# Optimization experiments

Hardware: AMD Instinct MI355X
Metric: run time of the kernel (lower is better)

Reference implementation:

```python
import jax, jax.numpy as jnp
import numpy as np

N = 8192
DIMS = 128
HID = 64
NEG = -9e15


def setup_inputs() -> dict:
    key = jax.random.key(0)
    k_adj, k_h, k_w1, k_w2 = jax.random.split(key, 4)
    graph_info = (jax.random.uniform(k_adj, (N, N)) < 0.01).astype(jnp.float32)
    h = jax.random.normal(k_h, (N, DIMS), dtype=jnp.float32)
    # xavier-normal-ish init for the 2-layer scoring MLP (dims -> 64 -> 1)
    W1 = jax.random.normal(k_w1, (DIMS, HID), dtype=jnp.float32) * np.sqrt(2.0 / (DIMS + HID))
    b1 = jnp.zeros((HID,), dtype=jnp.float32)
    W2 = jax.random.normal(k_w2, (HID, 1), dtype=jnp.float32) * np.sqrt(2.0 / (HID + 1))
    b2 = jnp.zeros((1,), dtype=jnp.float32)
    return {"graph_info": graph_info, "h": h, "W1": W1, "b1": b1, "W2": W2, "b2": b2}


def reference(graph_info, h, W1, b1, W2, b2):
    # per-node MLP score: e_j for every node j  -> [N, 1]
    e = jnp.dot(jnp.maximum(jnp.dot(h, W1) + b1, 0.0), W2) + b2
    # e.transpose().repeat(N,1): row i sees scores of all columns j -> broadcast [1, N]
    scores = e[:, 0][None, :]
    # mask non-edges with large negative, softmax over neighbors (dim=-1)
    att = jnp.where(graph_info > 0, scores, jnp.float32(NEG))
    att = jax.nn.softmax(att, axis=-1)
    out = jnp.dot(att, h)  # [N, dims] aggregation
    # sum_flag == 1: rescale each row by its degree (diagflat(num) @ h)
    num = jnp.sum(graph_info, axis=-1)  # [N]
    out = num[:, None] * out
    return out
```

## Files before the change

### kernel.cpp

```cpp
#include <hip/hip_runtime.h>
#include <math.h>

#define NN 8192
#define DIMS 128
#define HID 64
#define CAP 192

typedef float f4v __attribute__((ext_vector_type(4)));
typedef float f2v __attribute__((ext_vector_type(2)));

__global__ __launch_bounds__(256) void score_kernel(
    const float* __restrict__ h, const float* __restrict__ W1,
    const float* __restrict__ b1, const float* __restrict__ W2,
    const float* __restrict__ b2, float* __restrict__ e) {
  __shared__ float sW1[DIMS * HID];
  for (int i = threadIdx.x * 4; i < DIMS * HID; i += 1024)
    *(float4*)&sW1[i] = *(const float4*)&W1[i];
  __syncthreads();
  int wv = threadIdx.x >> 6, lane = threadIdx.x & 63;
  int j0 = blockIdx.x * 16 + wv * 4;
  const float* h0 = h + (size_t)j0 * DIMS;
  float bb = b1[lane];
  float a0 = bb, a1 = bb, a2 = bb, a3 = bb;
#pragma unroll 4
  for (int d = 0; d < DIMS; ++d) {
    float wc = sW1[d * HID + lane];
    a0 = fmaf(h0[d], wc, a0);
    a1 = fmaf(h0[d + DIMS], wc, a1);
    a2 = fmaf(h0[d + 2 * DIMS], wc, a2);
    a3 = fmaf(h0[d + 3 * DIMS], wc, a3);
  }
  float w2 = W2[lane];
  float r0 = fmaxf(a0, 0.f) * w2, r1 = fmaxf(a1, 0.f) * w2;
  float r2 = fmaxf(a2, 0.f) * w2, r3 = fmaxf(a3, 0.f) * w2;
#pragma unroll
  for (int off = 32; off > 0; off >>= 1) {
    r0 += __shfl_xor(r0, off, 64);
    r1 += __shfl_xor(r1, off, 64);
    r2 += __shfl_xor(r2, off, 64);
    r3 += __shfl_xor(r3, off, 64);
  }
  if (lane == 0) {
    float bo = b2[0];
    e[j0] = r0 + bo; e[j0 + 1] = r1 + bo; e[j0 + 2] = r2 + bo; e[j0 + 3] = r3 + bo;
  }
}

__global__ __launch_bounds__(1024) void expmax_kernel(
    const float* __restrict__ e, float* __restrict__ ee) {
  __shared__ float wmax[16];
  int tid = threadIdx.x;
  float m = -INFINITY;
  for (int i = tid; i < NN; i += 1024) m = fmaxf(m, e[i]);
#pragma unroll
  for (int off = 32; off > 0; off >>= 1) m = fmaxf(m, __shfl_xor(m, off, 64));
  int wave = tid >> 6, lane = tid & 63;
  if (lane == 0) wmax[wave] = m;
  __syncthreads();
  m = wmax[0];
#pragma unroll
  for (int w = 1; w < 16; ++w) m = fmaxf(m, wmax[w]);
  for (int i = tid; i < NN; i += 1024) ee[i] = expf(e[i] - m);
}

#define PROC(v, it)                                                            \
  do {                                                                         \
    int col = ((it) * 64 + lane) * 4;                                          \
    unsigned long long m0 = __ballot(v.x > 0.f);                               \
    unsigned long long m1 = __ballot(v.y > 0.f);                               \
    unsigned long long m2 = __ballot(v.z > 0.f);                               \
    unsigned long long m3 = __ballot(v.w > 0.f);                               \
    if (v.x > 0.f) { int o = cnt + __popcll(m0 & lt); if (o < CAP) s_idx[w][o] = col; }     \
    cnt += (int)__popcll(m0);                                                  \
    if (v.y > 0.f) { int o = cnt + __popcll(m1 & lt); if (o < CAP) s_idx[w][o] = col + 1; } \
    cnt += (int)__popcll(m1);                                                  \
    if (v.z > 0.f) { int o = cnt + __popcll(m2 & lt); if (o < CAP) s_idx[w][o] = col + 2; } \
    cnt += (int)__popcll(m2);                                                  \
    if (v.w > 0.f) { int o = cnt + __popcll(m3 & lt); if (o < CAP) s_idx[w][o] = col + 3; } \
    cnt += (int)__popcll(m3);                                                  \
  } while (0)

#define HLD(wj) (*(const float2*)(hbase + ((size_t)__float_as_int((wj).y)) * DIMS))

__global__ __launch_bounds__(256, 6) void agg_kernel(
    const float* __restrict__ graph, const float* __restrict__ h,
    const float* __restrict__ ee, float* __restrict__ out) {
  __shared__ int s_idx[4][CAP];
  __shared__ float2 s_wj[4][CAP];
  int w = threadIdx.x >> 6;
  int lane = threadIdx.x & 63;
  int row = blockIdx.x * 4 + w;
  const f4v* g4 = (const f4v*)(graph + (size_t)row * NN);
  unsigned long long lt = (1ull << lane) - 1ull;
  int cnt = 0;

  f4v c0 = __builtin_nontemporal_load(g4 + 0 * 64 + lane);
  f4v c1 = __builtin_nontemporal_load(g4 + 1 * 64 + lane);
  f4v c2 = __builtin_nontemporal_load(g4 + 2 * 64 + lane);
  f4v c3 = __builtin_nontemporal_load(g4 + 3 * 64 + lane);
#pragma unroll 1
  for (int it4 = 0; it4 < 8; ++it4) {
    f4v n0, n1, n2, n3;
    if (it4 < 7) {
      const f4v* nb = g4 + (it4 * 4 + 4) * 64 + lane;
      n0 = __builtin_nontemporal_load(nb);
      n1 = __builtin_nontemporal_load(nb + 64);
      n2 = __builtin_nontemporal_load(nb + 128);
      n3 = __builtin_nontemporal_load(nb + 192);
    } else {
      n0 = n1 = n2 = n3 = (f4v)(0.f);
    }
    PROC(c0, it4 * 4 + 0);
    PROC(c1, it4 * 4 + 1);
    PROC(c2, it4 * 4 + 2);
    PROC(c3, it4 * 4 + 3);
    c0 = n0; c1 = n1; c2 = n2; c3 = n3;
  }
  int count = cnt < CAP ? cnt : CAP;

  float z = 0.f;
  for (int q = lane; q < count; q += 64) {
    int j = s_idx[w][q];
    float wv = ee[j];
    s_wj[w][q] = make_float2(wv, __int_as_float(j));
    z += wv;
  }
#pragma unroll
  for (int off = 32; off > 0; off >>= 1) z += __shfl_xor(z, off, 64);

  float ax = 0.f, ay = 0.f;
  const float* hbase = h + lane * 2;
  int q = 0;
  int n8 = count & ~7;
  for (; q < n8; q += 8) {
    float2 wj0 = s_wj[w][q + 0], wj1 = s_wj[w][q + 1];
    float2 wj2 = s_wj[w][q + 2], wj3 = s_wj[w][q + 3];
    float2 wj4 = s_wj[w][q + 4], wj5 = s_wj[w][q + 5];
    float2 wj6 = s_wj[w][q + 6], wj7 = s_wj[w][q + 7];
    float2 h0 = HLD(wj0), h1 = HLD(wj1), h2 = HLD(wj2), h3 = HLD(wj3);
    float2 h4 = HLD(wj4), h5 = HLD(wj5), h6 = HLD(wj6), h7 = HLD(wj7);
    ax = fmaf(wj0.x, h0.x, ax); ay = fmaf(wj0.x, h0.y, ay);
    ax = fmaf(wj1.x, h1.x, ax); ay = fmaf(wj1.x, h1.y, ay);
    ax = fmaf(wj2.x, h2.x, ax); ay = fmaf(wj2.x, h2.y, ay);
    ax = fmaf(wj3.x, h3.x, ax); ay = fmaf(wj3.x, h3.y, ay);
    ax = fmaf(wj4.x, h4.x, ax); ay = fmaf(wj4.x, h4.y, ay);
    ax = fmaf(wj5.x, h5.x, ax); ay = fmaf(wj5.x, h5.y, ay);
    ax = fmaf(wj6.x, h6.x, ax); ay = fmaf(wj6.x, h6.y, ay);
    ax = fmaf(wj7.x, h7.x, ax); ay = fmaf(wj7.x, h7.y, ay);
  }
  for (; q < count; ++q) {
    float2 wj = s_wj[w][q];
    float2 hv = HLD(wj);
    ax = fmaf(wj.x, hv.x, ax);
    ay = fmaf(wj.x, hv.y, ay);
  }
  float scale = (count > 0) ? ((float)count / z) : 0.f;
  f2v o2;
  o2.x = ax * scale;
  o2.y = ay * scale;
  __builtin_nontemporal_store(o2, (f2v*)(out + (size_t)row * DIMS + lane * 2));
}

extern "C" void kernel_launch(void* const* d_in, const int* in_sizes, int n_in,
                              void* d_out, int out_size, void* d_ws, size_t ws_size,
                              hipStream_t stream) {
  const float* graph = (const float*)d_in[0];
  const float* h     = (const float*)d_in[1];
  const float* W1    = (const float*)d_in[2];
  const float* b1    = (const float*)d_in[3];
  const float* W2    = (const float*)d_in[4];
  const float* b2    = (const float*)d_in[5];
  float* out = (float*)d_out;
  float* e   = (float*)d_ws;
  float* ee  = e + NN;

  score_kernel<<<NN / 16, 256, 0, stream>>>(h, W1, b1, W2, b2, e);
  expmax_kernel<<<1, 1024, 0, stream>>>(e, ee);
  agg_kernel<<<NN / 4, 256, 0, stream>>>(graph, h, ee, out);
}
```

Measured before the change: 83.20 us.

## Drop global-max pass and split aggregation into compact and gather kernels

Removes the single-block max/exp kernel and computes exp(score) directly in the score kernel, relying on softmax shift-invariance and on the scores being small enough not to overflow. The aggregation kernel is split in two: a compact kernel scans the dense adjacency and writes 16-bit neighbor indices and counts to global workspace, and a gather kernel then does the weighted h aggregation. The goal is to drop the serial single-block kernel and let the bandwidth-bound scan run with more occupancy, separate from the gather. The cost is an extra launch, a global round-trip for the indices, and a risk of overflow in the unshifted exp.

New measurement: 88.99 us. +7.0%, slower.

```diff
diff --git a/kernel.cpp b/kernel.cpp
--- a/kernel.cpp
+++ b/kernel.cpp
@@ -12,7 +12,7 @@
 __global__ __launch_bounds__(256) void score_kernel(
     const float* __restrict__ h, const float* __restrict__ W1,
     const float* __restrict__ b1, const float* __restrict__ W2,
-    const float* __restrict__ b2, float* __restrict__ e) {
+    const float* __restrict__ b2, float* __restrict__ ee) {
   __shared__ float sW1[DIMS * HID];
   for (int i = threadIdx.x * 4; i < DIMS * HID; i += 1024)
     *(float4*)&sW1[i] = *(const float4*)&W1[i];
@@ -42,55 +42,38 @@
   }
   if (lane == 0) {
     float bo = b2[0];
-    e[j0] = r0 + bo; e[j0 + 1] = r1 + bo; e[j0 + 2] = r2 + bo; e[j0 + 3] = r3 + bo;
+    ee[j0]     = expf(r0 + bo);
+    ee[j0 + 1] = expf(r1 + bo);
+    ee[j0 + 2] = expf(r2 + bo);
+    ee[j0 + 3] = expf(r3 + bo);
   }
 }
 
-__global__ __launch_bounds__(1024) void expmax_kernel(
-    const float* __restrict__ e, float* __restrict__ ee) {
-  __shared__ float wmax[16];
-  int tid = threadIdx.x;
-  float m = -INFINITY;
-  for (int i = tid; i < NN; i += 1024) m = fmaxf(m, e[i]);
-#pragma unroll
-  for (int off = 32; off > 0; off >>= 1) m = fmaxf(m, __shfl_xor(m, off, 64));
-  int wave = tid >> 6, lane = tid & 63;
-  if (lane == 0) wmax[wave] = m;
-  __syncthreads();
-  m = wmax[0];
-#pragma unroll
-  for (int w = 1; w < 16; ++w) m = fmaxf(m, wmax[w]);
-  for (int i = tid; i < NN; i += 1024) ee[i] = expf(e[i] - m);
-}
-
-#define PROC(v, it)                                                            \
-  do {                                                                         \
-    int col = ((it) * 64 + lane) * 4;                                          \
-    unsigned long long m0 = __ballot(v.x > 0.f);                               \
-    unsigned long long m1 = __ballot(v.y > 0.f);                               \
-    unsigned long long m2 = __ballot(v.z > 0.f);                               \
-    unsigned long long m3 = __ballot(v.w > 0.f);                               \
-    if (v.x > 0.f) { int o = cnt + __popcll(m0 & lt); if (o < CAP) s_idx[w][o] = col; }     \
-    cnt += (int)__popcll(m0);                                                  \
-    if (v.y > 0.f) { int o = cnt + __popcll(m1 & lt); if (o < CAP) s_idx[w][o] = col + 1; } \
-    cnt += (int)__popcll(m1);                                                  \
-    if (v.z > 0.f) { int o = cnt + __popcll(m2 & lt); if (o < CAP) s_idx[w][o] = col + 2; } \
-    cnt += (int)__popcll(m2);                                                  \
-    if (v.w > 0.f) { int o = cnt + __popcll(m3 & lt); if (o < CAP) s_idx[w][o] = col + 3; } \
-    cnt += (int)__popcll(m3);                                                  \
+#define PROC(v, it)                                                                      \
+  do {                                                                                   \
+    int col = ((it) * 64 + lane) * 4;                                                    \
+    unsigned long long m0 = __ballot(v.x > 0.f);                                         \
+    unsigned long long m1 = __ballot(v.y > 0.f);                                         \
+    unsigned long long m2 = __ballot(v.z > 0.f);                                         \
+    unsigned long long m3 = __ballot(v.w > 0.f);                                         \
+    if (v.x > 0.f) { int o = cnt + __popcll(m0 & lt); if (o < CAP) rowidx[o] = (unsigned short)col; }       \
+    cnt += (int)__popcll(m0);                                                            \
+    if (v.y > 0.f) { int o = cnt + __popcll(m1 & lt); if (o < CAP) rowidx[o] = (unsigned short)(col + 1); } \
+    cnt += (int)__popcll(m1);                                                            \
+    if (v.z > 0.f) { int o = cnt + __popcll(m2 & lt); if (o < CAP) rowidx[o] = (unsigned short)(col + 2); } \
+    cnt += (int)__popcll(m2);                                                            \
+    if (v.w > 0.f) { int o = cnt + __popcll(m3 & lt); if (o < CAP) rowidx[o] = (unsigned short)(col + 3); } \
+    cnt += (int)__popcll(m3);                                                            \
   } while (0)
 
-#define HLD(wj) (*(const float2*)(hbase + ((size_t)__float_as_int((wj).y)) * DIMS))
-
-__global__ __launch_bounds__(256, 6) void agg_kernel(
-    const float* __restrict__ graph, const float* __restrict__ h,
-    const float* __restrict__ ee, float* __restrict__ out) {
-  __shared__ int s_idx[4][CAP];
-  __shared__ float2 s_wj[4][CAP];
+__global__ __launch_bounds__(256) void compact_kernel(
+    const float* __restrict__ graph, unsigned short* __restrict__ idx16,
+    int* __restrict__ counts) {
   int w = threadIdx.x >> 6;
   int lane = threadIdx.x & 63;
   int row = blockIdx.x * 4 + w;
   const f4v* g4 = (const f4v*)(graph + (size_t)row * NN);
+  unsigned short* rowidx = idx16 + (size_t)row * CAP;
   unsigned long long lt = (1ull << lane) - 1ull;
   int cnt = 0;
 
@@ -116,11 +99,25 @@
     PROC(c3, it4 * 4 + 3);
     c0 = n0; c1 = n1; c2 = n2; c3 = n3;
   }
-  int count = cnt < CAP ? cnt : CAP;
+  if (lane == 0) counts[row] = cnt < CAP ? cnt : CAP;
+}
+
+#define HLD(wj) (*(const float2*)(hbase + ((size_t)__float_as_int((wj).y)) * DIMS))
+
+__global__ __launch_bounds__(256) void gather_kernel(
+    const unsigned short* __restrict__ idx16, const int* __restrict__ counts,
+    const float* __restrict__ ee, const float* __restrict__ h,
+    float* __restrict__ out) {
+  __shared__ float2 s_wj[4][CAP];
+  int w = threadIdx.x >> 6;
+  int lane = threadIdx.x & 63;
+  int row = blockIdx.x * 4 + w;
+  int count = counts[row];
+  const unsigned short* rowidx = idx16 + (size_t)row * CAP;
 
   float z = 0.f;
   for (int q = lane; q < count; q += 64) {
-    int j = s_idx[w][q];
+    int j = rowidx[q];
     float wv = ee[j];
     s_wj[w][q] = make_float2(wv, __int_as_float(j));
     z += wv;
@@ -171,10 +168,12 @@
   const float* W2    = (const float*)d_in[4];
   const float* b2    = (const float*)d_in[5];
   float* out = (float*)d_out;
-  float* e   = (float*)d_ws;
-  float* ee  = e + NN;
 
-  score_kernel<<<NN / 16, 256, 0, stream>>>(h, W1, b1, W2, b2, e);
-  expmax_kernel<<<1, 1024, 0, stream>>>(e, ee);
-  agg_kernel<<<NN / 4, 256, 0, stream>>>(graph, h, ee, out);
+  float* ee = (float*)d_ws;
+  int* counts = (int*)((char*)d_ws + NN * sizeof(float));
+  unsigned short* idx16 = (unsigned short*)((char*)d_ws + NN * (sizeof(float) + sizeof(int)));
+
+  score_kernel<<<NN / 16, 256, 0, stream>>>(h, W1, b1, W2, b2, ee);
+  compact_kernel<<<NN / 4, 256, 0, stream>>>(graph, idx16, counts);
+  gather_kernel<<<NN / 4, 256, 0, stream>>>(idx16, counts, ee, h, out);
 }
```
